# Kernel tuning notes

Measured on AMD Instinct MI355X. Metric: run time of the kernel, lower is better.

## Reference

```python
import jax, jax.numpy as jnp
import numpy as np

N_NODES = 100000
N_EDGES = 1600000
NUM_PROP = 5
CAT_PROP = 3
INPUT_DIM = 128
HIDDEN = 128
NUM_REL = 2


def setup_inputs() -> dict:
    key = jax.random.key(0)
    ks = jax.random.split(key, 20)
    s = 0.05
    inp = {
        "x": jax.random.normal(ks[0], (N_NODES, NUM_PROP + CAT_PROP), jnp.float32),
        "edge_index": jax.random.randint(ks[1], (2, N_EDGES), 0, N_NODES, jnp.int64 if jax.config.jax_enable_x64 else jnp.int32),
        "edge_type": jax.random.randint(ks[2], (N_EDGES,), 0, NUM_REL, jnp.int32),
        # numeric / categorical encoders -> input_dim/2 each
        "W_num": jax.random.normal(ks[3], (NUM_PROP, INPUT_DIM // 2), jnp.float32) * s,
        "b_num": jnp.zeros((INPUT_DIM // 2,), jnp.float32),
        "W_cat": jax.random.normal(ks[4], (CAT_PROP, INPUT_DIM // 2), jnp.float32) * s,
        "b_cat": jnp.zeros((INPUT_DIM // 2,), jnp.float32),
        # input projection + PReLU
        "W_in": jax.random.normal(ks[5], (INPUT_DIM, HIDDEN), jnp.float32) * s,
        "b_in": jnp.zeros((HIDDEN,), jnp.float32),
        "prelu_a": jnp.full((HIDDEN,), 0.25, jnp.float32),
        # RGCN layer 1
        "W_rel1": jax.random.normal(ks[6], (NUM_REL, HIDDEN, HIDDEN), jnp.float32) * s,
        "W_root1": jax.random.normal(ks[7], (HIDDEN, HIDDEN), jnp.float32) * s,
        "b_rgcn1": jnp.zeros((HIDDEN,), jnp.float32),
        # RGCN layer 2
        "W_rel2": jax.random.normal(ks[8], (NUM_REL, HIDDEN, HIDDEN), jnp.float32) * s,
        "W_root2": jax.random.normal(ks[9], (HIDDEN, HIDDEN), jnp.float32) * s,
        "b_rgcn2": jnp.zeros((HIDDEN,), jnp.float32),
        # classifier (single Linear)
        "W_cls": jax.random.normal(ks[10], (HIDDEN, HIDDEN), jnp.float32) * s,
        "b_cls": jnp.zeros((HIDDEN,), jnp.float32),
    }
    return inp


def _leaky_relu(x, slope=0.01):
    return jnp.where(x >= 0, x, slope * x)


def _prelu(x, a):
    return jnp.where(x >= 0, x, a * x)


def _rgcn_conv(x, edge_index, edge_type, W_rel, W_root, bias):
    # PyG RGCNConv: out[i] = x[i] @ W_root + bias + sum_r mean_{j in N_r(i)} x[j] @ W_r
    # Aggregate-then-transform (linearity) to avoid per-edge (E, d) @ W products.
    src, dst = edge_index[0], edge_index[1]
    n = x.shape[0]
    x_src = x[src]  # (E, d) gather
    out = x @ W_root + bias
    for r in range(W_rel.shape[0]):
        w = (edge_type == r).astype(x.dtype)  # (E,)
        agg = jax.ops.segment_sum(x_src * w[:, None], dst, num_segments=n)  # (N, d)
        deg = jax.ops.segment_sum(w, dst, num_segments=n)  # (N,)
        out = out + (agg / jnp.clip(deg, 1.0)[:, None]) @ W_rel[r]
    return out


def reference(x, edge_index, edge_type, W_num, b_num, W_cat, b_cat, W_in, b_in,
              prelu_a, W_rel1, W_root1, b_rgcn1, W_rel2, W_root2, b_rgcn2,
              W_cls, b_cls):
    num_prop = x[:, :NUM_PROP]
    cat_prop = x[:, NUM_PROP:NUM_PROP + CAT_PROP]
    n = _leaky_relu(num_prop @ W_num + b_num)
    c = _leaky_relu(cat_prop @ W_cat + b_cat)
    h = jnp.concatenate([n, c], axis=1)
    h = _prelu(h @ W_in + b_in, prelu_a)
    h = _rgcn_conv(h, edge_index, edge_type, W_rel1, W_root1, b_rgcn1)
    # dropout is identity in eval mode
    h = _rgcn_conv(h, edge_index, edge_type, W_rel2, W_root2, b_rgcn2)
    return h @ W_cls + b_cls
```

## Files before the change

### kernel.cpp

```cpp
#include <hip/hip_runtime.h>
#include <cstdint>


typedef short bf16x8 __attribute__((ext_vector_type(8)));
typedef float f32x4  __attribute__((ext_vector_type(4)));

__device__ __forceinline__ unsigned short f2bf(float f) {
    unsigned int u = __builtin_bit_cast(unsigned int, f);
    u += 0x7fff + ((u >> 16) & 1);
    return (unsigned short)(u >> 16);
}
__device__ __forceinline__ float bf2f(unsigned short h) {
    unsigned int u = ((unsigned int)h) << 16;
    return __builtin_bit_cast(float, u);
}
__device__ __forceinline__ float lo16f(unsigned int u) {
    return __builtin_bit_cast(float, u << 16);
}
__device__ __forceinline__ float hi16f(unsigned int u) {
    return __builtin_bit_cast(float, u & 0xffff0000u);
}

__device__ __forceinline__ void gload_lds16(const void* g, void* l) {
    __builtin_amdgcn_global_load_lds(
        (const __attribute__((address_space(1))) void*)g,
        (__attribute__((address_space(3))) void*)l, 16, 0, 0);
}

__global__ __launch_bounds__(256) void k_egemm(
    const float* __restrict__ x,
    const float* __restrict__ Wnum, const float* __restrict__ bnum,
    const float* __restrict__ Wcat, const float* __restrict__ bcat,
    const unsigned short* __restrict__ Bhi, const unsigned short* __restrict__ Blo,
    const float* __restrict__ bias, const float* __restrict__ prelu,
    unsigned short* __restrict__ C_hi, unsigned short* __restrict__ C_lo, int M)
{
    __shared__ unsigned short lds[2][16 * 512];
    const int t = threadIdx.x;
    const int w = t >> 6, lane = t & 63;
    const int laneL = lane & 15, laneH = lane >> 4;
    const int wi = w >> 1, wj = w & 1;
    const int m0 = blockIdx.x * 128;
    const int Mm1 = M - 1;

    f32x4 acc[4][4];
    #pragma unroll
    for (int a = 0; a < 4; ++a)
        #pragma unroll
        for (int b = 0; b < 4; ++b)
            acc[a][b] = (f32x4){0.f, 0.f, 0.f, 0.f};

    auto stage = [&](int s, unsigned short* buf) {
        int koff = s * 32;
        int k8 = koff + laneH * 8;
        #pragma unroll
        for (int c = 0; c < 2; ++c) {
            int j = w + c * 4;
            int rc = j * 16 + laneL;
            int row = (m0 + rc <= Mm1) ? (m0 + rc) : Mm1;
            const float4* xr = (const float4*)(x + (size_t)row * 8);
            float4 X0 = xr[0], X1 = xr[1];
            float a[8];
            if (k8 < 64) {
                const float4* bp = (const float4*)(bnum + k8);
                float4 b0 = bp[0], b1 = bp[1];
                a[0]=b0.x; a[1]=b0.y; a[2]=b0.z; a[3]=b0.w;
                a[4]=b1.x; a[5]=b1.y; a[6]=b1.z; a[7]=b1.w;
                float xs0 = X0.x, xs1 = X0.y, xs2 = X0.z, xs3 = X0.w, xs4 = X1.x;
                const float* wb = Wnum + k8;
                #pragma unroll
                for (int p = 0; p < 5; ++p) {
                    float xp = p==0?xs0 : p==1?xs1 : p==2?xs2 : p==3?xs3 : xs4;
                    const float4* wp = (const float4*)(wb + p * 64);
                    float4 w0 = wp[0], w1 = wp[1];
                    a[0]+=xp*w0.x; a[1]+=xp*w0.y; a[2]+=xp*w0.z; a[3]+=xp*w0.w;
                    a[4]+=xp*w1.x; a[5]+=xp*w1.y; a[6]+=xp*w1.z; a[7]+=xp*w1.w;
                }
            } else {
                int kk = k8 - 64;
                const float4* bp = (const float4*)(bcat + kk);
                float4 b0 = bp[0], b1 = bp[1];
                a[0]=b0.x; a[1]=b0.y; a[2]=b0.z; a[3]=b0.w;
                a[4]=b1.x; a[5]=b1.y; a[6]=b1.z; a[7]=b1.w;
                float xs0 = X1.y, xs1 = X1.z, xs2 = X1.w;
                const float* wb = Wcat + kk;
                #pragma unroll
                for (int p = 0; p < 3; ++p) {
                    float xp = p==0?xs0 : p==1?xs1 : xs2;
                    const float4* wp = (const float4*)(wb + p * 64);
                    float4 w0 = wp[0], w1 = wp[1];
                    a[0]+=xp*w0.x; a[1]+=xp*w0.y; a[2]+=xp*w0.z; a[3]+=xp*w0.w;
                    a[4]+=xp*w1.x; a[5]+=xp*w1.y; a[6]+=xp*w1.z; a[7]+=xp*w1.w;
                }
            }
            unsigned hw[4], lw[4];
            #pragma unroll
            for (int q = 0; q < 4; ++q) {
                float v0 = a[2*q]   >= 0.f ? a[2*q]   : 0.01f * a[2*q];
                float v1 = a[2*q+1] >= 0.f ? a[2*q+1] : 0.01f * a[2*q+1];
                unsigned short h0 = f2bf(v0), h1 = f2bf(v1);
                unsigned short l0 = f2bf(v0 - bf2f(h0)), l1 = f2bf(v1 - bf2f(h1));
                hw[q] = (unsigned)h0 | ((unsigned)h1 << 16);
                lw[q] = (unsigned)l0 | ((unsigned)l1 << 16);
            }
            uint4 ho, lo_;
            ho.x=hw[0]; ho.y=hw[1]; ho.z=hw[2]; ho.w=hw[3];
            lo_.x=lw[0]; lo_.y=lw[1]; lo_.z=lw[2]; lo_.w=lw[3];
            *(uint4*)&buf[(0 * 8 + j) * 512 + lane * 8] = ho;
            *(uint4*)&buf[(8 + j) * 512 + lane * 8] = lo_;
        }
    };

    stage(0, lds[0]);
    for (int s = 0; s < 4; ++s) {
        unsigned short* cur = lds[s & 1];
        unsigned short* nxt = lds[(s & 1) ^ 1];
        __syncthreads();
        if (s + 1 < 4) stage(s + 1, nxt);
        int koff = s * 32;
        const bf16x8* fr = (const bf16x8*)cur;
        bf16x8 ah[4], al[4], bh[4], bl[4];
        #pragma unroll
        for (int mi = 0; mi < 4; ++mi) {
            ah[mi] = fr[(0 + wi * 4 + mi) * 64 + lane];
            al[mi] = fr[(8 + wi * 4 + mi) * 64 + lane];
        }
        #pragma unroll
        for (int nj = 0; nj < 4; ++nj) {
            size_t boff = (size_t)(wj * 64 + nj * 16 + laneL) * 128 + koff + laneH * 8;
            bh[nj] = *(const bf16x8*)(Bhi + boff);
            bl[nj] = *(const bf16x8*)(Blo + boff);
        }
        #pragma unroll
        for (int mi = 0; mi < 4; ++mi)
            #pragma unroll
            for (int nj = 0; nj < 4; ++nj) {
                acc[mi][nj] = __builtin_amdgcn_mfma_f32_16x16x32_bf16(
                    ah[mi], bh[nj], acc[mi][nj], 0, 0, 0);
                acc[mi][nj] = __builtin_amdgcn_mfma_f32_16x16x32_bf16(
                    ah[mi], bl[nj], acc[mi][nj], 0, 0, 0);
                acc[mi][nj] = __builtin_amdgcn_mfma_f32_16x16x32_bf16(
                    al[mi], bh[nj], acc[mi][nj], 0, 0, 0);
            }
    }

    float bv[4], av[4];
    #pragma unroll
    for (int nj = 0; nj < 4; ++nj) {
        int col = wj * 64 + nj * 16 + laneL;
        bv[nj] = bias[col];
        av[nj] = prelu[col];
    }
    unsigned short* lp = &lds[0][0];
    #pragma unroll
    for (int pass = 0; pass < 2; ++pass) {
        __syncthreads();
        #pragma unroll
        for (int nj = 0; nj < 4; ++nj) {
            int col = wj * 64 + nj * 16 + laneL;
            #pragma unroll
            for (int mi = 0; mi < 4; ++mi)
                #pragma unroll
                for (int r = 0; r < 4; ++r) {
                    int row = wi * 64 + mi * 16 + laneH * 4 + r;
                    float v = acc[mi][nj][r] + bv[nj];
                    v = v >= 0.f ? v : av[nj] * v;
                    unsigned short h = f2bf(v);
                    lp[row * 128 + col] = pass == 0 ? h : f2bf(v - bf2f(h));
                }
        }
        __syncthreads();
        unsigned short* dst = pass == 0 ? C_hi : C_lo;
        const uint4* lsrc = (const uint4*)lp;
        #pragma unroll
        for (int it = 0; it < 8; ++it) {
            int idx = it * 256 + t;
            int row = idx >> 4, c = idx & 15;
            int m = m0 + row;
            if (m < M)
                ((uint4*)(dst + (size_t)m * 128))[c] = lsrc[idx];
        }
    }
}

struct WHArgs {
    const float* W[8];
    unsigned short* hi[8];
    unsigned short* lo[8];
    const int* ei;
    const int* et;
    int* cntmatT;
    int E;
    int N;
    int NBINS;
};
__global__ __launch_bounds__(256) void k_wsplit_hist(WHArgs a)
{
    __shared__ int hist[1024];
    const int t = threadIdx.x;
    const int b = blockIdx.x;
    if (b < 512) {
        int part = b >> 6;
        int idx = (b & 63) * 256 + t;
        int n = idx >> 7, k = idx & 127;
        float v = a.W[part][(size_t)k * 128 + n];
        unsigned short h = f2bf(v);
        a.hi[part][(size_t)n * 128 + k] = h;
        a.lo[part][(size_t)n * 128 + k] = f2bf(v - bf2f(h));
        return;
    }
    const int blk = b - 512;
    for (int i = t; i < a.NBINS; i += 256) hist[i] = 0;
    __syncthreads();
    #pragma unroll
    for (int j = 0; j < 16; ++j) {
        int e = blk * 4096 + j * 256 + t;
        if (e < a.E) atomicAdd(&hist[(a.et[e] * a.N + a.ei[a.E + e]) >> 8], 1);
    }
    __syncthreads();
    for (int i = t; i < a.NBINS; i += 256)
        a.cntmatT[(size_t)blk * a.NBINS + i] = hist[i];
}

__global__ __launch_bounds__(256) void k_transpose(
    const int* __restrict__ src, int* __restrict__ dst, int R, int C)
{
    __shared__ int tile[32][33];
    int ctiles = (C + 31) >> 5;
    int bx = blockIdx.x % ctiles;
    int by = blockIdx.x / ctiles;
    int tc = threadIdx.x & 31, tr = threadIdx.x >> 5;
    int c0 = bx * 32, r0 = by * 32;
    #pragma unroll
    for (int i = 0; i < 32; i += 8) {
        int r = r0 + tr + i, c = c0 + tc;
        if (r < R && c < C) tile[tr + i][tc] = src[(size_t)r * C + c];
    }
    __syncthreads();
    #pragma unroll
    for (int i = 0; i < 32; i += 8) {
        int r = r0 + tc;
        int c = c0 + tr + i;
        if (r < R && c < C) dst[(size_t)c * R + r] = tile[tc][tr + i];
    }
}

__global__ __launch_bounds__(256) void k_transpose_add(
    const int* __restrict__ src, int* __restrict__ dst,
    const int* __restrict__ bsum, int R, int C)
{
    __shared__ int tile[32][33];
    int ctiles = (C + 31) >> 5;
    int bx = blockIdx.x % ctiles;
    int by = blockIdx.x / ctiles;
    int tc = threadIdx.x & 31, tr = threadIdx.x >> 5;
    int c0 = bx * 32, r0 = by * 32;
    #pragma unroll
    for (int i = 0; i < 32; i += 8) {
        int r = r0 + tr + i, c = c0 + tc;
        if (r < R && c < C) {
            size_t idx = (size_t)r * C + c;
            tile[tr + i][tc] = src[idx] + bsum[idx >> 8];
        }
    }
    __syncthreads();
    #pragma unroll
    for (int i = 0; i < 32; i += 8) {
        int r = r0 + tc;
        int c = c0 + tr + i;
        if (r < R && c < C) dst[(size_t)c * R + r] = tile[tc][tr + i];
    }
}

__global__ __launch_bounds__(256) void k_scan1(
    const int* __restrict__ src, int* __restrict__ dst,
    int* __restrict__ bsum, int n)
{
    __shared__ int s[256];
    int t = threadIdx.x;
    int i = blockIdx.x * 256 + t;
    int v = (i < n) ? src[i] : 0;
    s[t] = v;
    __syncthreads();
    #pragma unroll
    for (int d = 1; d < 256; d <<= 1) {
        int add = (t >= d) ? s[t - d] : 0;
        __syncthreads();
        s[t] += add;
        __syncthreads();
    }
    if (i < n) dst[i] = s[t] - v;
    if (t == 255) bsum[blockIdx.x] = s[255];
}

__global__ __launch_bounds__(1024) void k_scan2(int* __restrict__ bsum, int nb)
{
    __shared__ int s[1024];
    int t = threadIdx.x;
    int carry = 0;
    for (int base = 0; base < nb; base += 1024) {
        int i = base + t;
        int v = (i < nb) ? bsum[i] : 0;
        s[t] = v;
        __syncthreads();
        #pragma unroll
        for (int d = 1; d < 1024; d <<= 1) {
            int add = (t >= d) ? s[t - d] : 0;
            __syncthreads();
            s[t] += add;
            __syncthreads();
        }
        if (i < nb) bsum[i] = carry + s[t] - v;
        carry += s[1023];
        __syncthreads();
    }
}

__global__ __launch_bounds__(256) void k_binscatter(
    const int* __restrict__ ei, const int* __restrict__ et,
    const int* __restrict__ cntscanT, int* __restrict__ ebuf,
    int E, int N, int NBINS)
{
    __shared__ int base[1024];
    const int t = threadIdx.x;
    const int blk = blockIdx.x;
    for (int i = t; i < NBINS; i += 256)
        base[i] = cntscanT[(size_t)blk * NBINS + i];
    __syncthreads();
    #pragma unroll
    for (int j = 0; j < 16; ++j) {
        int e = blk * 4096 + j * 256 + t;
        if (e < E) {
            unsigned src = (unsigned)ei[e];
            int seg = et[e] * N + ei[E + e];
            int pos = atomicAdd(&base[seg >> 8], 1);
            ebuf[pos] = (int)(((unsigned)(seg & 255) << 24) | src);
        }
    }
}

__global__ __launch_bounds__(256) void k_bincsr(
    const int* __restrict__ cntscan, const int* __restrict__ bsum,
    const int* __restrict__ ebuf,
    int* __restrict__ deg, int* __restrict__ off, int* __restrict__ esrc,
    int E, int nseg, int NBLK, int NBINS)
{
    __shared__ int cnt[256];
    __shared__ int pfx[256];
    __shared__ int cur[256];
    const int b = blockIdx.x;
    const int t = threadIdx.x;
    size_t i0 = (size_t)b * NBLK;
    const int est = cntscan[i0] + bsum[i0 >> 8];
    int een = E;
    if (b + 1 < NBINS) {
        size_t i1 = (size_t)(b + 1) * NBLK;
        een = cntscan[i1] + bsum[i1 >> 8];
    }
    cnt[t] = 0;
    __syncthreads();
    for (int e = est + t; e < een; e += 256)
        atomicAdd(&cnt[((unsigned)ebuf[e]) >> 24], 1);
    __syncthreads();
    int v = cnt[t];
    pfx[t] = v;
    __syncthreads();
    #pragma unroll
    for (int d = 1; d < 256; d <<= 1) {
        int add = (t >= d) ? pfx[t - d] : 0;
        __syncthreads();
        pfx[t] += add;
        __syncthreads();
    }
    int o = est + pfx[t] - v;
    int seg = b * 256 + t;
    if (seg < nseg) { deg[seg] = v; off[seg] = o; }
    cur[t] = o;
    __syncthreads();
    for (int e = est + t; e < een; e += 256) {
        unsigned u = (unsigned)ebuf[e];
        int p = atomicAdd(&cur[u >> 24], 1);
        esrc[p] = (int)(u & 0xffffffu);
    }
}

__global__ __launch_bounds__(256) void k_gather(
    const unsigned short* __restrict__ h_hi,
    const int* __restrict__ esrc,
    const int* __restrict__ off, const int* __restrict__ deg,
    unsigned short* __restrict__ a_hi, int nseg)
{
    int i = blockIdx.x * 8 + (threadIdx.x >> 5);
    if (i >= nseg) return;
    int l32 = threadIdx.x & 31;
    int q = l32 >> 4;
    int l16 = l32 & 15;
    int cnt = deg[i], st = off[i];
    const uint4* hp = (const uint4*)h_hi;
    float a0 = 0.f, a1 = 0.f, a2 = 0.f, a3 = 0.f;
    float a4 = 0.f, a5 = 0.f, a6 = 0.f, a7 = 0.f;
    int e = q;
    for (; e + 6 < cnt; e += 8) {
        int i0 = esrc[st + e + 0];
        int i1 = esrc[st + e + 2];
        int i2 = esrc[st + e + 4];
        int i3 = esrc[st + e + 6];
        uint4 u0 = hp[(size_t)i0 * 16 + l16];
        uint4 u1 = hp[(size_t)i1 * 16 + l16];
        uint4 u2 = hp[(size_t)i2 * 16 + l16];
        uint4 u3 = hp[(size_t)i3 * 16 + l16];
        a0 += lo16f(u0.x); a1 += hi16f(u0.x); a2 += lo16f(u0.y); a3 += hi16f(u0.y);
        a4 += lo16f(u0.z); a5 += hi16f(u0.z); a6 += lo16f(u0.w); a7 += hi16f(u0.w);
        a0 += lo16f(u1.x); a1 += hi16f(u1.x); a2 += lo16f(u1.y); a3 += hi16f(u1.y);
        a4 += lo16f(u1.z); a5 += hi16f(u1.z); a6 += lo16f(u1.w); a7 += hi16f(u1.w);
        a0 += lo16f(u2.x); a1 += hi16f(u2.x); a2 += lo16f(u2.y); a3 += hi16f(u2.y);
        a4 += lo16f(u2.z); a5 += hi16f(u2.z); a6 += lo16f(u2.w); a7 += hi16f(u2.w);
        a0 += lo16f(u3.x); a1 += hi16f(u3.x); a2 += lo16f(u3.y); a3 += hi16f(u3.y);
        a4 += lo16f(u3.z); a5 += hi16f(u3.z); a6 += lo16f(u3.w); a7 += hi16f(u3.w);
    }
    for (; e < cnt; e += 2) {
        uint4 u = hp[(size_t)esrc[st + e] * 16 + l16];
        a0 += lo16f(u.x); a1 += hi16f(u.x); a2 += lo16f(u.y); a3 += hi16f(u.y);
        a4 += lo16f(u.z); a5 += hi16f(u.z); a6 += lo16f(u.w); a7 += hi16f(u.w);
    }
    a0 += __shfl_xor(a0, 16, 64);
    a1 += __shfl_xor(a1, 16, 64);
    a2 += __shfl_xor(a2, 16, 64);
    a3 += __shfl_xor(a3, 16, 64);
    a4 += __shfl_xor(a4, 16, 64);
    a5 += __shfl_xor(a5, 16, 64);
    a6 += __shfl_xor(a6, 16, 64);
    a7 += __shfl_xor(a7, 16, 64);
    if (q == 0) {
        float inv = 1.0f / (float)(cnt > 1 ? cnt : 1);
        uint4 o;
        o.x = (unsigned int)f2bf(a0 * inv) | ((unsigned int)f2bf(a1 * inv) << 16);
        o.y = (unsigned int)f2bf(a2 * inv) | ((unsigned int)f2bf(a3 * inv) << 16);
        o.z = (unsigned int)f2bf(a4 * inv) | ((unsigned int)f2bf(a5 * inv) << 16);
        o.w = (unsigned int)f2bf(a6 * inv) | ((unsigned int)f2bf(a7 * inv) << 16);
        ((uint4*)a_hi)[(size_t)i * 16 + l16] = o;
    }
}

struct GArgs {
    const unsigned short* A_hi[3];
    const unsigned short* A_lo[3];
    const unsigned short* B_hi[3];
    const unsigned short* B_lo[3];
    int alo[3];
    int blo[3];
    const float* bias;
    unsigned short* C_hi;
    unsigned short* C_lo;
    int M;
    int P;
    const unsigned short* clsBhi;
    const unsigned short* clsBlo;
    const float* clsBias;
    float* outF;
};

__global__ __launch_bounds__(256) void k_mgemm(GArgs g)
{
    __shared__ unsigned short lds[2][16 * 512];
    const int t = threadIdx.x;
    const int w = t >> 6, lane = t & 63;
    const int laneL = lane & 15, laneH = lane >> 4;
    const int wi = w >> 1, wj = w & 1;
    const int m0 = blockIdx.x * 128;
    const int Mm1 = g.M - 1;
    const int S = g.P * 4;

    f32x4 acc[4][4];
    #pragma unroll
    for (int a = 0; a < 4; ++a)
        #pragma unroll
        for (int b = 0; b < 4; ++b)
            acc[a][b] = (f32x4){0.f, 0.f, 0.f, 0.f};

    auto stage = [&](int s, unsigned short* buf) {
        int p = s >> 2, koff = (s & 3) * 32;
        const unsigned short* tpA[2];
        tpA[0] = g.A_hi[p];
        tpA[1] = g.alo[p] ? g.A_lo[p] : nullptr;
        #pragma unroll
        for (int c = 0; c < 4; ++c) {
            int chunk = w + c * 4;
            int slot = chunk >> 3, j = chunk & 7;
            const unsigned short* plane = tpA[slot];
            if (!plane) continue;
            int rc = j * 16 + laneL;
            int row = (m0 + rc <= Mm1) ? (m0 + rc) : Mm1;
            gload_lds16(plane + (size_t)row * 128 + koff + laneH * 8,
                        &buf[(slot * 8 + j) * 512]);
        }
    };

    stage(0, lds[0]);
    for (int s = 0; s < S; ++s) {
        unsigned short* cur = lds[s & 1];
        unsigned short* nxt = lds[(s & 1) ^ 1];
        __syncthreads();
        if (s + 1 < S) stage(s + 1, nxt);
        int p = s >> 2, koff = (s & 3) * 32;
        const bool hasAlo = g.alo[p] != 0;
        const bool hasBlo = g.blo[p] != 0;
        const bf16x8* fr = (const bf16x8*)cur;
        bf16x8 ah[4], al[4], bh[4], bl[4];
        #pragma unroll
        for (int mi = 0; mi < 4; ++mi)
            ah[mi] = fr[(0 + wi * 4 + mi) * 64 + lane];
        if (hasAlo) {
            #pragma unroll
            for (int mi = 0; mi < 4; ++mi)
                al[mi] = fr[(8 + wi * 4 + mi) * 64 + lane];
        }
        const unsigned short* Bh = g.B_hi[p];
        const unsigned short* Bl = g.B_lo[p];
        #pragma unroll
        for (int nj = 0; nj < 4; ++nj) {
            size_t boff = (size_t)(wj * 64 + nj * 16 + laneL) * 128 + koff + laneH * 8;
            bh[nj] = *(const bf16x8*)(Bh + boff);
            if (hasBlo) bl[nj] = *(const bf16x8*)(Bl + boff);
        }
        #pragma unroll
        for (int mi = 0; mi < 4; ++mi)
            #pragma unroll
            for (int nj = 0; nj < 4; ++nj) {
                acc[mi][nj] = __builtin_amdgcn_mfma_f32_16x16x32_bf16(
                    ah[mi], bh[nj], acc[mi][nj], 0, 0, 0);
                if (hasBlo)
                    acc[mi][nj] = __builtin_amdgcn_mfma_f32_16x16x32_bf16(
                        ah[mi], bl[nj], acc[mi][nj], 0, 0, 0);
                if (hasAlo)
                    acc[mi][nj] = __builtin_amdgcn_mfma_f32_16x16x32_bf16(
                        al[mi], bh[nj], acc[mi][nj], 0, 0, 0);
            }
    }

    float bv[4];
    #pragma unroll
    for (int nj = 0; nj < 4; ++nj)
        bv[nj] = g.bias[wj * 64 + nj * 16 + laneL];
    unsigned short* lp = &lds[0][0];
    #pragma unroll
    for (int pass = 0; pass < 2; ++pass) {
        __syncthreads();
        #pragma unroll
        for (int nj = 0; nj < 4; ++nj) {
            int col = wj * 64 + nj * 16 + laneL;
            #pragma unroll
            for (int mi = 0; mi < 4; ++mi)
                #pragma unroll
                for (int r = 0; r < 4; ++r) {
                    int row = wi * 64 + mi * 16 + laneH * 4 + r;
                    float v = acc[mi][nj][r] + bv[nj];
                    unsigned short h = f2bf(v);
                    lp[row * 128 + col] = pass == 0 ? h : f2bf(v - bf2f(h));
                }
        }
        __syncthreads();
        unsigned short* dst = pass == 0 ? g.C_hi : g.C_lo;
        const uint4* lsrc = (const uint4*)lp;
        #pragma unroll
        for (int it = 0; it < 8; ++it) {
            int idx = it * 256 + t;
            int row = idx >> 4, c = idx & 15;
            int m = m0 + row;
            if (m < g.M)
                ((uint4*)(dst + (size_t)m * 128))[c] = lsrc[idx];
        }
    }
}

__global__ __launch_bounds__(256) void k_mgemm_cls(GArgs g)
{
    __shared__ unsigned short lds[2][16 * 512];
    const int t = threadIdx.x;
    const int w = t >> 6, lane = t & 63;
    const int laneL = lane & 15, laneH = lane >> 4;
    const int wi = w >> 1, wj = w & 1;
    const int m0 = blockIdx.x * 128;
    const int Mm1 = g.M - 1;
    const int S = g.P * 4;

    f32x4 acc[4][4];
    #pragma unroll
    for (int a = 0; a < 4; ++a)
        #pragma unroll
        for (int b = 0; b < 4; ++b)
            acc[a][b] = (f32x4){0.f, 0.f, 0.f, 0.f};

    auto stage = [&](int s, unsigned short* buf) {
        int p = s >> 2, koff = (s & 3) * 32;
        const unsigned short* tpA[2];
        tpA[0] = g.A_hi[p];
        tpA[1] = g.alo[p] ? g.A_lo[p] : nullptr;
        #pragma unroll
        for (int c = 0; c < 4; ++c) {
            int chunk = w + c * 4;
            int slot = chunk >> 3, j = chunk & 7;
            const unsigned short* plane = tpA[slot];
            if (!plane) continue;
            int rc = j * 16 + laneL;
            int row = (m0 + rc <= Mm1) ? (m0 + rc) : Mm1;
            gload_lds16(plane + (size_t)row * 128 + koff + laneH * 8,
                        &buf[(slot * 8 + j) * 512]);
        }
    };

    stage(0, lds[0]);
    for (int s = 0; s < S; ++s) {
        unsigned short* cur = lds[s & 1];
        unsigned short* nxt = lds[(s & 1) ^ 1];
        __syncthreads();
        if (s + 1 < S) stage(s + 1, nxt);
        int p = s >> 2, koff = (s & 3) * 32;
        const bool hasAlo = g.alo[p] != 0;
        const bool hasBlo = g.blo[p] != 0;
        const bf16x8* fr = (const bf16x8*)cur;
        bf16x8 ah[4], al[4], bh[4], bl[4];
        #pragma unroll
        for (int mi = 0; mi < 4; ++mi)
            ah[mi] = fr[(0 + wi * 4 + mi) * 64 + lane];
        if (hasAlo) {
            #pragma unroll
            for (int mi = 0; mi < 4; ++mi)
                al[mi] = fr[(8 + wi * 4 + mi) * 64 + lane];
        }
        const unsigned short* Bh = g.B_hi[p];
        const unsigned short* Bl = g.B_lo[p];
        #pragma unroll
        for (int nj = 0; nj < 4; ++nj) {
            size_t boff = (size_t)(wj * 64 + nj * 16 + laneL) * 128 + koff + laneH * 8;
            bh[nj] = *(const bf16x8*)(Bh + boff);
            if (hasBlo) bl[nj] = *(const bf16x8*)(Bl + boff);
        }
        #pragma unroll
        for (int mi = 0; mi < 4; ++mi)
            #pragma unroll
            for (int nj = 0; nj < 4; ++nj) {
                acc[mi][nj] = __builtin_amdgcn_mfma_f32_16x16x32_bf16(
                    ah[mi], bh[nj], acc[mi][nj], 0, 0, 0);
                if (hasBlo)
                    acc[mi][nj] = __builtin_amdgcn_mfma_f32_16x16x32_bf16(
                        ah[mi], bl[nj], acc[mi][nj], 0, 0, 0);
                if (hasAlo)
                    acc[mi][nj] = __builtin_amdgcn_mfma_f32_16x16x32_bf16(
                        al[mi], bh[nj], acc[mi][nj], 0, 0, 0);
            }
    }

    float bv[4];
    #pragma unroll
    for (int nj = 0; nj < 4; ++nj)
        bv[nj] = g.bias[wj * 64 + nj * 16 + laneL];

    char* pl = (char*)&lds[0][0];
    unsigned lopack[4][4][2];

    __syncthreads();
    #pragma unroll
    for (int nj = 0; nj < 4; ++nj) {
        int col = wj * 64 + nj * 16 + laneL;
        #pragma unroll
        for (int mi = 0; mi < 4; ++mi)
            #pragma unroll
            for (int r = 0; r < 4; ++r) {
                int row = wi * 64 + mi * 16 + laneH * 4 + r;
                float v = acc[mi][nj][r] + bv[nj];
                unsigned short h = f2bf(v);
                unsigned short l = f2bf(v - bf2f(h));
                int offb = row * 256 + ((col * 2) ^ ((row & 7) << 4));
                *(unsigned short*)(pl + offb) = h;
                if (r & 1) lopack[nj][mi][r >> 1] |= (unsigned)l << 16;
                else       lopack[nj][mi][r >> 1] = l;
            }
    }
    __syncthreads();

    f32x4 acc2[4][4];
    #pragma unroll
    for (int a = 0; a < 4; ++a)
        #pragma unroll
        for (int b = 0; b < 4; ++b)
            acc2[a][b] = (f32x4){0.f, 0.f, 0.f, 0.f};

    #pragma unroll
    for (int ks = 0; ks < 4; ++ks) {
        bf16x8 ah2[4], bh2[4], bl2[4];
        #pragma unroll
        for (int mi = 0; mi < 4; ++mi) {
            int rc = wi * 64 + mi * 16 + laneL;
            int aoff = rc * 256 + ((ks * 64 + laneH * 16) ^ ((rc & 7) << 4));
            ah2[mi] = *(const bf16x8*)(pl + aoff);
        }
        #pragma unroll
        for (int nj = 0; nj < 4; ++nj) {
            size_t boff = (size_t)(wj * 64 + nj * 16 + laneL) * 128 + ks * 32 + laneH * 8;
            bh2[nj] = *(const bf16x8*)(g.clsBhi + boff);
            bl2[nj] = *(const bf16x8*)(g.clsBlo + boff);
        }
        #pragma unroll
        for (int mi = 0; mi < 4; ++mi)
            #pragma unroll
            for (int nj = 0; nj < 4; ++nj) {
                acc2[mi][nj] = __builtin_amdgcn_mfma_f32_16x16x32_bf16(
                    ah2[mi], bh2[nj], acc2[mi][nj], 0, 0, 0);
                acc2[mi][nj] = __builtin_amdgcn_mfma_f32_16x16x32_bf16(
                    ah2[mi], bl2[nj], acc2[mi][nj], 0, 0, 0);
            }
    }
    __syncthreads();

    #pragma unroll
    for (int nj = 0; nj < 4; ++nj) {
        int col = wj * 64 + nj * 16 + laneL;
        #pragma unroll
        for (int mi = 0; mi < 4; ++mi)
            #pragma unroll
            for (int r = 0; r < 4; ++r) {
                int row = wi * 64 + mi * 16 + laneH * 4 + r;
                unsigned short l = (r & 1) ? (unsigned short)(lopack[nj][mi][r >> 1] >> 16)
                                           : (unsigned short)(lopack[nj][mi][r >> 1] & 0xffff);
                int offb = row * 256 + ((col * 2) ^ ((row & 7) << 4));
                *(unsigned short*)(pl + offb) = l;
            }
    }
    __syncthreads();

    #pragma unroll
    for (int ks = 0; ks < 4; ++ks) {
        bf16x8 al2[4], bh2[4];
        #pragma unroll
        for (int mi = 0; mi < 4; ++mi) {
            int rc = wi * 64 + mi * 16 + laneL;
            int aoff = rc * 256 + ((ks * 64 + laneH * 16) ^ ((rc & 7) << 4));
            al2[mi] = *(const bf16x8*)(pl + aoff);
        }
        #pragma unroll
        for (int nj = 0; nj < 4; ++nj) {
            size_t boff = (size_t)(wj * 64 + nj * 16 + laneL) * 128 + ks * 32 + laneH * 8;
            bh2[nj] = *(const bf16x8*)(g.clsBhi + boff);
        }
        #pragma unroll
        for (int mi = 0; mi < 4; ++mi)
            #pragma unroll
            for (int nj = 0; nj < 4; ++nj)
                acc2[mi][nj] = __builtin_amdgcn_mfma_f32_16x16x32_bf16(
                    al2[mi], bh2[nj], acc2[mi][nj], 0, 0, 0);
    }

    float cb[4];
    #pragma unroll
    for (int nj = 0; nj < 4; ++nj)
        cb[nj] = g.clsBias[wj * 64 + nj * 16 + laneL];
    float* lf = (float*)&lds[0][0];
    #pragma unroll
    for (int half = 0; half < 2; ++half) {
        __syncthreads();
        if (wi == half) {
            #pragma unroll
            for (int nj = 0; nj < 4; ++nj) {
                int col = wj * 64 + nj * 16 + laneL;
                #pragma unroll
                for (int mi = 0; mi < 4; ++mi)
                    #pragma unroll
                    for (int r = 0; r < 4; ++r) {
                        int lrow = mi * 16 + laneH * 4 + r;
                        lf[lrow * 128 + col] = acc2[mi][nj][r] + cb[nj];
                    }
            }
        }
        __syncthreads();
        const uint4* lsrc = (const uint4*)lf;
        #pragma unroll
        for (int it = 0; it < 8; ++it) {
            int idx = it * 256 + t;
            int row = idx >> 5, c = idx & 31;
            int m = m0 + half * 64 + row;
            if (m < g.M)
                ((uint4*)(g.outF + (size_t)m * 128))[c] = lsrc[idx];
        }
    }
}

extern "C" void kernel_launch(void* const* d_in, const int* in_sizes, int n_in,
                              void* d_out, int out_size, void* d_ws, size_t ws_size,
                              hipStream_t stream) {
    const float* x      = (const float*)d_in[0];
    const int*   ei     = (const int*)d_in[1];
    const int*   et     = (const int*)d_in[2];
    const float* Wnum   = (const float*)d_in[3];
    const float* bnum   = (const float*)d_in[4];
    const float* Wcat   = (const float*)d_in[5];
    const float* bcat   = (const float*)d_in[6];
    const float* Win    = (const float*)d_in[7];
    const float* bin    = (const float*)d_in[8];
    const float* pa     = (const float*)d_in[9];
    const float* Wrel1  = (const float*)d_in[10];
    const float* Wroot1 = (const float*)d_in[11];
    const float* brg1   = (const float*)d_in[12];
    const float* Wrel2  = (const float*)d_in[13];
    const float* Wroot2 = (const float*)d_in[14];
    const float* brg2   = (const float*)d_in[15];
    const float* Wcls   = (const float*)d_in[16];
    const float* bcls   = (const float*)d_in[17];
    float* out = (float*)d_out;

    const int N = in_sizes[0] / 8;
    const int E = in_sizes[1] / 2;
    const int nseg = 2 * N;
    const size_t NH = (size_t)N * 128;

    const int NBLK  = (E + 4095) / 4096;
    const int NBINS = (nseg + 255) / 256;
    const long long L = (long long)NBINS * NBLK;

    char* w = (char*)d_ws;
    unsigned short* h1_hi = (unsigned short*)w;  w += NH * 2;
    unsigned short* h1_lo = (unsigned short*)w;  w += NH * 2;
    unsigned short* agg_hi = (unsigned short*)w; w += 2 * NH * 2;
    int* deg      = (int*)w;  w += (size_t)nseg * 4;
    int* off      = (int*)w;  w += (size_t)nseg * 4;
    int* cntmatT  = (int*)w;  w += (size_t)L * 4;
    int* cntmat   = (int*)w;  w += (size_t)L * 4;
    int* cntscan  = (int*)w;  w += (size_t)L * 4;
    int* cntscanT = (int*)w;  w += (size_t)L * 4;
    int* esrc     = (int*)w;  w += (size_t)E * 4;
    int* bsum     = (int*)w;  w += 4096 * 4;
    unsigned short* wplanes = (unsigned short*)w;  w += 8 * 2 * 16384 * 2;

    int* ebuf = (int*)d_out;
    unsigned short* h0_hi = (unsigned short*)d_out;
    unsigned short* h0_lo = h0_hi + NH;

    unsigned short* whi[8];
    unsigned short* wlo[8];
    for (int i = 0; i < 8; ++i) {
        whi[i] = wplanes + (size_t)i * 2 * 16384;
        wlo[i] = whi[i] + 16384;
    }

    const int gm = (N + 127) / 128;
    const int gg = (nseg + 7) / 8;

    {
        WHArgs a;
        a.W[0] = Win;   a.W[1] = Wroot1; a.W[2] = Wrel1; a.W[3] = Wrel1 + 16384;
        a.W[4] = Wroot2; a.W[5] = Wrel2; a.W[6] = Wrel2 + 16384; a.W[7] = Wcls;
        for (int i = 0; i < 8; ++i) { a.hi[i] = whi[i]; a.lo[i] = wlo[i]; }
        a.ei = ei; a.et = et; a.cntmatT = cntmatT;
        a.E = E; a.N = N; a.NBINS = NBINS;
        k_wsplit_hist<<<512 + NBLK, 256, 0, stream>>>(a);
    }

    k_transpose<<<((NBLK + 31) / 32) * ((NBINS + 31) / 32), 256, 0, stream>>>(
        cntmatT, cntmat, NBLK, NBINS);

    const int nb1 = (int)((L + 255) / 256);
    k_scan1<<<nb1, 256, 0, stream>>>(cntmat, cntscan, bsum, (int)L);
    k_scan2<<<1, 1024, 0, stream>>>(bsum, nb1);
    k_transpose_add<<<((NBINS + 31) / 32) * ((NBLK + 31) / 32), 256, 0, stream>>>(
        cntscan, cntscanT, bsum, NBINS, NBLK);

    k_binscatter<<<NBLK, 256, 0, stream>>>(ei, et, cntscanT, ebuf, E, N, NBINS);
    k_bincsr<<<NBINS, 256, 0, stream>>>(cntscan, bsum, ebuf, deg, off, esrc,
                                        E, nseg, NBLK, NBINS);

    k_egemm<<<gm, 256, 0, stream>>>(x, Wnum, bnum, Wcat, bcat,
                                    whi[0], wlo[0], bin, pa,
                                    h0_hi, h0_lo, N);

    k_gather<<<gg, 256, 0, stream>>>(h0_hi, esrc, off, deg, agg_hi, nseg);
    {
        GArgs g = {};
        g.A_hi[0] = h0_hi;       g.A_lo[0] = h0_lo;  g.alo[0] = 1; g.blo[0] = 1;
        g.A_hi[1] = agg_hi;      g.alo[1] = 0;       g.blo[1] = 0;
        g.A_hi[2] = agg_hi + NH; g.alo[2] = 0;       g.blo[2] = 0;
        g.B_hi[0] = whi[1]; g.B_lo[0] = wlo[1];
        g.B_hi[1] = whi[2]; g.B_lo[1] = wlo[2];
        g.B_hi[2] = whi[3]; g.B_lo[2] = wlo[3];
        g.bias = brg1;
        g.C_hi = h1_hi; g.C_lo = h1_lo;
        g.M = N; g.P = 3;
        k_mgemm<<<gm, 256, 0, stream>>>(g);
    }
    k_gather<<<gg, 256, 0, stream>>>(h1_hi, esrc, off, deg, agg_hi, nseg);
    {
        GArgs g = {};
        g.A_hi[0] = h1_hi;       g.A_lo[0] = h1_lo;  g.alo[0] = 1; g.blo[0] = 1;
        g.A_hi[1] = agg_hi;      g.alo[1] = 0;       g.blo[1] = 0;
        g.A_hi[2] = agg_hi + NH; g.alo[2] = 0;       g.blo[2] = 0;
        g.B_hi[0] = whi[4]; g.B_lo[0] = wlo[4];
        g.B_hi[1] = whi[5]; g.B_lo[1] = wlo[5];
        g.B_hi[2] = whi[6]; g.B_lo[2] = wlo[6];
        g.bias = brg2;
        g.M = N; g.P = 3;
        g.clsBhi = whi[7]; g.clsBlo = wlo[7];
        g.clsBias = bcls; g.outF = out;
        k_mgemm_cls<<<gm, 256, 0, stream>>>(g);
    }
}
```

Baseline: 518.5 us.

## Stage B weight tiles through LDS and drop A-tile double buffering in GEMMs

Each GEMM kernel now copies the B (weight) hi/lo tiles into shared memory with global_load_lds, alongside the A tiles, and reads MFMA B fragments from LDS rather than directly from global memory. To fit the larger single buffer, the double-buffered prefetch of the next K-step is removed, so each step loads, synchronizes, then computes. This is meant to replace per-wave strided global B reads with one cooperative load per block, but it gives up the overlap between loading and compute.

```diff
diff --git a/kernel.cpp b/kernel.cpp
--- a/kernel.cpp
+++ b/kernel.cpp
@@ -35,7 +35,7 @@
     const float* __restrict__ bias, const float* __restrict__ prelu,
     unsigned short* __restrict__ C_hi, unsigned short* __restrict__ C_lo, int M)
 {
-    __shared__ unsigned short lds[2][16 * 512];
+    __shared__ unsigned short lds[32 * 512];
     const int t = threadIdx.x;
     const int w = t >> 6, lane = t & 63;
     const int laneL = lane & 15, laneH = lane >> 4;
@@ -50,75 +50,80 @@
         for (int b = 0; b < 4; ++b)
             acc[a][b] = (f32x4){0.f, 0.f, 0.f, 0.f};
 
-    auto stage = [&](int s, unsigned short* buf) {
+    for (int s = 0; s < 4; ++s) {
         int koff = s * 32;
-        int k8 = koff + laneH * 8;
-        #pragma unroll
-        for (int c = 0; c < 2; ++c) {
-            int j = w + c * 4;
+        __syncthreads();
+        {
+            int k8 = koff + laneH * 8;
+            #pragma unroll
+            for (int c = 0; c < 2; ++c) {
+                int j = w + c * 4;
+                int rc = j * 16 + laneL;
+                int row = (m0 + rc <= Mm1) ? (m0 + rc) : Mm1;
+                const float4* xr = (const float4*)(x + (size_t)row * 8);
+                float4 X0 = xr[0], X1 = xr[1];
+                float a[8];
+                if (k8 < 64) {
+                    const float4* bp = (const float4*)(bnum + k8);
+                    float4 b0 = bp[0], b1 = bp[1];
+                    a[0]=b0.x; a[1]=b0.y; a[2]=b0.z; a[3]=b0.w;
+                    a[4]=b1.x; a[5]=b1.y; a[6]=b1.z; a[7]=b1.w;
+                    float xs0 = X0.x, xs1 = X0.y, xs2 = X0.z, xs3 = X0.w, xs4 = X1.x;
+                    const float* wb = Wnum + k8;
+                    #pragma unroll
+                    for (int p = 0; p < 5; ++p) {
+                        float xp = p==0?xs0 : p==1?xs1 : p==2?xs2 : p==3?xs3 : xs4;
+                        const float4* wp = (const float4*)(wb + p * 64);
+                        float4 w0 = wp[0], w1 = wp[1];
+                        a[0]+=xp*w0.x; a[1]+=xp*w0.y; a[2]+=xp*w0.z; a[3]+=xp*w0.w;
+                        a[4]+=xp*w1.x; a[5]+=xp*w1.y; a[6]+=xp*w1.z; a[7]+=xp*w1.w;
+                    }
+                } else {
+                    int kk = k8 - 64;
+                    const float4* bp = (const float4*)(bcat + kk);
+                    float4 b0 = bp[0], b1 = bp[1];
+                    a[0]=b0.x; a[1]=b0.y; a[2]=b0.z; a[3]=b0.w;
+                    a[4]=b1.x; a[5]=b1.y; a[6]=b1.z; a[7]=b1.w;
+                    float xs0 = X1.y, xs1 = X1.z, xs2 = X1.w;
+                    const float* wb = Wcat + kk;
+                    #pragma unroll
+                    for (int p = 0; p < 3; ++p) {
+                        float xp = p==0?xs0 : p==1?xs1 : xs2;
+                        const float4* wp = (const float4*)(wb + p * 64);
+                        float4 w0 = wp[0], w1 = wp[1];
+                        a[0]+=xp*w0.x; a[1]+=xp*w0.y; a[2]+=xp*w0.z; a[3]+=xp*w0.w;
+                        a[4]+=xp*w1.x; a[5]+=xp*w1.y; a[6]+=xp*w1.z; a[7]+=xp*w1.w;
+                    }
+                }
+                unsigned hw[4], lw[4];
+                #pragma unroll
+                for (int q = 0; q < 4; ++q) {
+                    float v0 = a[2*q]   >= 0.f ? a[2*q]   : 0.01f * a[2*q];
+                    float v1 = a[2*q+1] >= 0.f ? a[2*q+1] : 0.01f * a[2*q+1];
+                    unsigned short h0 = f2bf(v0), h1 = f2bf(v1);
+                    unsigned short l0 = f2bf(v0 - bf2f(h0)), l1 = f2bf(v1 - bf2f(h1));
+                    hw[q] = (unsigned)h0 | ((unsigned)h1 << 16);
+                    lw[q] = (unsigned)l0 | ((unsigned)l1 << 16);
+                }
+                uint4 ho, lo_;
+                ho.x=hw[0]; ho.y=hw[1]; ho.z=hw[2]; ho.w=hw[3];
+                lo_.x=lw[0]; lo_.y=lw[1]; lo_.z=lw[2]; lo_.w=lw[3];
+                *(uint4*)&lds[(0 * 8 + j) * 512 + lane * 8] = ho;
+                *(uint4*)&lds[(8 + j) * 512 + lane * 8] = lo_;
+            }
+        }
+        #pragma unroll
+        for (int c = 4; c < 8; ++c) {
+            int chunk = w + c * 4;
+            int slot = chunk >> 3, j = chunk & 7;
+            const unsigned short* plane = (slot == 2) ? Bhi : Blo;
             int rc = j * 16 + laneL;
-            int row = (m0 + rc <= Mm1) ? (m0 + rc) : Mm1;
-            const float4* xr = (const float4*)(x + (size_t)row * 8);
-            float4 X0 = xr[0], X1 = xr[1];
-            float a[8];
-            if (k8 < 64) {
-                const float4* bp = (const float4*)(bnum + k8);
-                float4 b0 = bp[0], b1 = bp[1];
-                a[0]=b0.x; a[1]=b0.y; a[2]=b0.z; a[3]=b0.w;
-                a[4]=b1.x; a[5]=b1.y; a[6]=b1.z; a[7]=b1.w;
-                float xs0 = X0.x, xs1 = X0.y, xs2 = X0.z, xs3 = X0.w, xs4 = X1.x;
-                const float* wb = Wnum + k8;
-                #pragma unroll
-                for (int p = 0; p < 5; ++p) {
-                    float xp = p==0?xs0 : p==1?xs1 : p==2?xs2 : p==3?xs3 : xs4;
-                    const float4* wp = (const float4*)(wb + p * 64);
-                    float4 w0 = wp[0], w1 = wp[1];
-                    a[0]+=xp*w0.x; a[1]+=xp*w0.y; a[2]+=xp*w0.z; a[3]+=xp*w0.w;
-                    a[4]+=xp*w1.x; a[5]+=xp*w1.y; a[6]+=xp*w1.z; a[7]+=xp*w1.w;
-                }
-            } else {
-                int kk = k8 - 64;
-                const float4* bp = (const float4*)(bcat + kk);
-                float4 b0 = bp[0], b1 = bp[1];
-                a[0]=b0.x; a[1]=b0.y; a[2]=b0.z; a[3]=b0.w;
-                a[4]=b1.x; a[5]=b1.y; a[6]=b1.z; a[7]=b1.w;
-                float xs0 = X1.y, xs1 = X1.z, xs2 = X1.w;
-                const float* wb = Wcat + kk;
-                #pragma unroll
-                for (int p = 0; p < 3; ++p) {
-                    float xp = p==0?xs0 : p==1?xs1 : xs2;
-                    const float4* wp = (const float4*)(wb + p * 64);
-                    float4 w0 = wp[0], w1 = wp[1];
-                    a[0]+=xp*w0.x; a[1]+=xp*w0.y; a[2]+=xp*w0.z; a[3]+=xp*w0.w;
-                    a[4]+=xp*w1.x; a[5]+=xp*w1.y; a[6]+=xp*w1.z; a[7]+=xp*w1.w;
-                }
-            }
-            unsigned hw[4], lw[4];
-            #pragma unroll
-            for (int q = 0; q < 4; ++q) {
-                float v0 = a[2*q]   >= 0.f ? a[2*q]   : 0.01f * a[2*q];
-                float v1 = a[2*q+1] >= 0.f ? a[2*q+1] : 0.01f * a[2*q+1];
-                unsigned short h0 = f2bf(v0), h1 = f2bf(v1);
-                unsigned short l0 = f2bf(v0 - bf2f(h0)), l1 = f2bf(v1 - bf2f(h1));
-                hw[q] = (unsigned)h0 | ((unsigned)h1 << 16);
-                lw[q] = (unsigned)l0 | ((unsigned)l1 << 16);
-            }
-            uint4 ho, lo_;
-            ho.x=hw[0]; ho.y=hw[1]; ho.z=hw[2]; ho.w=hw[3];
-            lo_.x=lw[0]; lo_.y=lw[1]; lo_.z=lw[2]; lo_.w=lw[3];
-            *(uint4*)&buf[(0 * 8 + j) * 512 + lane * 8] = ho;
-            *(uint4*)&buf[(8 + j) * 512 + lane * 8] = lo_;
-        }
-    };
-
-    stage(0, lds[0]);
-    for (int s = 0; s < 4; ++s) {
-        unsigned short* cur = lds[s & 1];
-        unsigned short* nxt = lds[(s & 1) ^ 1];
-        __syncthreads();
-        if (s + 1 < 4) stage(s + 1, nxt);
-        int koff = s * 32;
-        const bf16x8* fr = (const bf16x8*)cur;
+            gload_lds16(plane + (size_t)rc * 128 + koff + laneH * 8,
+                        &lds[(slot * 8 + j) * 512]);
+        }
+        __syncthreads();
+
+        const bf16x8* fr = (const bf16x8*)lds;
         bf16x8 ah[4], al[4], bh[4], bl[4];
         #pragma unroll
         for (int mi = 0; mi < 4; ++mi) {
@@ -127,9 +132,8 @@
         }
         #pragma unroll
         for (int nj = 0; nj < 4; ++nj) {
-            size_t boff = (size_t)(wj * 64 + nj * 16 + laneL) * 128 + koff + laneH * 8;
-            bh[nj] = *(const bf16x8*)(Bhi + boff);
-            bl[nj] = *(const bf16x8*)(Blo + boff);
+            bh[nj] = fr[(16 + wj * 4 + nj) * 64 + lane];
+            bl[nj] = fr[(24 + wj * 4 + nj) * 64 + lane];
         }
         #pragma unroll
         for (int mi = 0; mi < 4; ++mi)
@@ -151,7 +155,7 @@
         bv[nj] = bias[col];
         av[nj] = prelu[col];
     }
-    unsigned short* lp = &lds[0][0];
+    unsigned short* lp = &lds[0];
     #pragma unroll
     for (int pass = 0; pass < 2; ++pass) {
         __syncthreads();
@@ -462,7 +466,7 @@
 
 __global__ __launch_bounds__(256) void k_mgemm(GArgs g)
 {
-    __shared__ unsigned short lds[2][16 * 512];
+    __shared__ unsigned short lds[32 * 512];
     const int t = threadIdx.x;
     const int w = t >> 6, lane = t & 63;
     const int laneL = lane & 15, laneH = lane >> 4;
@@ -478,34 +482,30 @@
         for (int b = 0; b < 4; ++b)
             acc[a][b] = (f32x4){0.f, 0.f, 0.f, 0.f};
 
-    auto stage = [&](int s, unsigned short* buf) {
+    for (int s = 0; s < S; ++s) {
         int p = s >> 2, koff = (s & 3) * 32;
-        const unsigned short* tpA[2];
-        tpA[0] = g.A_hi[p];
-        tpA[1] = g.alo[p] ? g.A_lo[p] : nullptr;
-        #pragma unroll
-        for (int c = 0; c < 4; ++c) {
+        const unsigned short* tp[4];
+        tp[0] = g.A_hi[p];
+        tp[1] = g.alo[p] ? g.A_lo[p] : nullptr;
+        tp[2] = g.B_hi[p];
+        tp[3] = g.blo[p] ? g.B_lo[p] : nullptr;
+        __syncthreads();
+        #pragma unroll
+        for (int c = 0; c < 8; ++c) {
             int chunk = w + c * 4;
             int slot = chunk >> 3, j = chunk & 7;
-            const unsigned short* plane = tpA[slot];
+            const unsigned short* plane = tp[slot];
             if (!plane) continue;
             int rc = j * 16 + laneL;
-            int row = (m0 + rc <= Mm1) ? (m0 + rc) : Mm1;
+            int row = (slot < 2) ? (m0 + rc <= Mm1 ? m0 + rc : Mm1) : rc;
             gload_lds16(plane + (size_t)row * 128 + koff + laneH * 8,
-                        &buf[(slot * 8 + j) * 512]);
-        }
-    };
-
-    stage(0, lds[0]);
-    for (int s = 0; s < S; ++s) {
-        unsigned short* cur = lds[s & 1];
-        unsigned short* nxt = lds[(s & 1) ^ 1];
-        __syncthreads();
-        if (s + 1 < S) stage(s + 1, nxt);
-        int p = s >> 2, koff = (s & 3) * 32;
+                        &lds[(slot * 8 + j) * 512]);
+        }
+        __syncthreads();
+
         const bool hasAlo = g.alo[p] != 0;
         const bool hasBlo = g.blo[p] != 0;
-        const bf16x8* fr = (const bf16x8*)cur;
+        const bf16x8* fr = (const bf16x8*)lds;
         bf16x8 ah[4], al[4], bh[4], bl[4];
         #pragma unroll
         for (int mi = 0; mi < 4; ++mi)
@@ -515,13 +515,13 @@
             for (int mi = 0; mi < 4; ++mi)
                 al[mi] = fr[(8 + wi * 4 + mi) * 64 + lane];
         }
-        const unsigned short* Bh = g.B_hi[p];
-        const unsigned short* Bl = g.B_lo[p];
-        #pragma unroll
-        for (int nj = 0; nj < 4; ++nj) {
-            size_t boff = (size_t)(wj * 64 + nj * 16 + laneL) * 128 + koff + laneH * 8;
-            bh[nj] = *(const bf16x8*)(Bh + boff);
-            if (hasBlo) bl[nj] = *(const bf16x8*)(Bl + boff);
+        #pragma unroll
+        for (int nj = 0; nj < 4; ++nj)
+            bh[nj] = fr[(16 + wj * 4 + nj) * 64 + lane];
+        if (hasBlo) {
+            #pragma unroll
+            for (int nj = 0; nj < 4; ++nj)
+                bl[nj] = fr[(24 + wj * 4 + nj) * 64 + lane];
         }
         #pragma unroll
         for (int mi = 0; mi < 4; ++mi)
@@ -542,7 +542,7 @@
     #pragma unroll
     for (int nj = 0; nj < 4; ++nj)
         bv[nj] = g.bias[wj * 64 + nj * 16 + laneL];
-    unsigned short* lp = &lds[0][0];
+    unsigned short* lp = &lds[0];
     #pragma unroll
     for (int pass = 0; pass < 2; ++pass) {
         __syncthreads();
@@ -575,7 +575,7 @@
 
 __global__ __launch_bounds__(256) void k_mgemm_cls(GArgs g)
 {
-    __shared__ unsigned short lds[2][16 * 512];
+    __shared__ unsigned short lds[32 * 512];
     const int t = threadIdx.x;
     const int w = t >> 6, lane = t & 63;
     const int laneL = lane & 15, laneH = lane >> 4;
@@ -591,34 +591,30 @@
         for (int b = 0; b < 4; ++b)
             acc[a][b] = (f32x4){0.f, 0.f, 0.f, 0.f};
 
-    auto stage = [&](int s, unsigned short* buf) {
+    for (int s = 0; s < S; ++s) {
         int p = s >> 2, koff = (s & 3) * 32;
-        const unsigned short* tpA[2];
-        tpA[0] = g.A_hi[p];
-        tpA[1] = g.alo[p] ? g.A_lo[p] : nullptr;
-        #pragma unroll
-        for (int c = 0; c < 4; ++c) {
+        const unsigned short* tp[4];
+        tp[0] = g.A_hi[p];
+        tp[1] = g.alo[p] ? g.A_lo[p] : nullptr;
+        tp[2] = g.B_hi[p];
+        tp[3] = g.blo[p] ? g.B_lo[p] : nullptr;
+        __syncthreads();
+        #pragma unroll
+        for (int c = 0; c < 8; ++c) {
             int chunk = w + c * 4;
             int slot = chunk >> 3, j = chunk & 7;
-            const unsigned short* plane = tpA[slot];
+            const unsigned short* plane = tp[slot];
             if (!plane) continue;
             int rc = j * 16 + laneL;
-            int row = (m0 + rc <= Mm1) ? (m0 + rc) : Mm1;
+            int row = (slot < 2) ? (m0 + rc <= Mm1 ? m0 + rc : Mm1) : rc;
             gload_lds16(plane + (size_t)row * 128 + koff + laneH * 8,
-                        &buf[(slot * 8 + j) * 512]);
-        }
-    };
-
-    stage(0, lds[0]);
-    for (int s = 0; s < S; ++s) {
-        unsigned short* cur = lds[s & 1];
-        unsigned short* nxt = lds[(s & 1) ^ 1];
-        __syncthreads();
-        if (s + 1 < S) stage(s + 1, nxt);
-        int p = s >> 2, koff = (s & 3) * 32;
+                        &lds[(slot * 8 + j) * 512]);
+        }
+        __syncthreads();
+
         const bool hasAlo = g.alo[p] != 0;
         const bool hasBlo = g.blo[p] != 0;
-        const bf16x8* fr = (const bf16x8*)cur;
+        const bf16x8* fr = (const bf16x8*)lds;
         bf16x8 ah[4], al[4], bh[4], bl[4];
         #pragma unroll
         for (int mi = 0; mi < 4; ++mi)
@@ -628,13 +624,13 @@
             for (int mi = 0; mi < 4; ++mi)
                 al[mi] = fr[(8 + wi * 4 + mi) * 64 + lane];
         }
-        const unsigned short* Bh = g.B_hi[p];
-        const unsigned short* Bl = g.B_lo[p];
-        #pragma unroll
-        for (int nj = 0; nj < 4; ++nj) {
-            size_t boff = (size_t)(wj * 64 + nj * 16 + laneL) * 128 + koff + laneH * 8;
-            bh[nj] = *(const bf16x8*)(Bh + boff);
-            if (hasBlo) bl[nj] = *(const bf16x8*)(Bl + boff);
+        #pragma unroll
+        for (int nj = 0; nj < 4; ++nj)
+            bh[nj] = fr[(16 + wj * 4 + nj) * 64 + lane];
+        if (hasBlo) {
+            #pragma unroll
+            for (int nj = 0; nj < 4; ++nj)
+                bl[nj] = fr[(24 + wj * 4 + nj) * 64 + lane];
         }
         #pragma unroll
         for (int mi = 0; mi < 4; ++mi)
@@ -656,7 +652,7 @@
     for (int nj = 0; nj < 4; ++nj)
         bv[nj] = g.bias[wj * 64 + nj * 16 + laneL];
 
-    char* pl = (char*)&lds[0][0];
+    char* pl = (char*)&lds[0];
     unsigned lopack[4][4][2];
 
     __syncthreads();
@@ -755,7 +751,7 @@
     #pragma unroll
     for (int nj = 0; nj < 4; ++nj)
         cb[nj] = g.clsBias[wj * 64 + nj * 16 + laneL];
-    float* lf = (float*)&lds[0][0];
+    float* lf = (float*)&lds[0];
     #pragma unroll
     for (int half = 0; half < 2; ++half) {
         __syncthreads();
```

New measurement: 505.4 us. 1.03x faster.
